# Kernel optimization log

Measured on AMD Instinct MI355X. Metric: run time of the kernel, lower is better.

## Reference

```python
import jax, jax.numpy as jnp
import numpy as np

N = 100000
E = 1600000
D_IN = 128
D_H = 128


def _logit(p):
    p = max(min(p, 0.999), 0.001)
    return float(np.log(p / (1.0 - p)))


def setup_inputs() -> dict:
    key = jax.random.key(0)
    ks = jax.random.split(key, 16)
    s = 0.05
    inp = {
        "x": jax.random.normal(ks[0], (N, D_IN), jnp.float32),
        "edge_index": jax.random.randint(ks[1], (2, E), 0, N, jnp.int64),
        "reranker_scores": jax.random.normal(ks[2], (N,), jnp.float32),
        # input_proj
        "Wp": jax.random.normal(ks[3], (D_IN, D_H), jnp.float32) * s,
        "bp": jnp.zeros((D_H,), jnp.float32),
        # SAGEConv 0: lin_l (on aggregated neighbors, has bias), lin_r (root, no bias)
        "Wl0": jax.random.normal(ks[4], (D_IN, D_H), jnp.float32) * s,
        "bl0": jnp.zeros((D_H,), jnp.float32),
        "Wr0": jax.random.normal(ks[5], (D_IN, D_H), jnp.float32) * s,
        # SAGEConv 1
        "Wl1": jax.random.normal(ks[6], (D_H, D_H), jnp.float32) * s,
        "bl1": jnp.zeros((D_H,), jnp.float32),
        "Wr1": jax.random.normal(ks[7], (D_H, D_H), jnp.float32) * s,
        # score head: Linear(128,64) -> GELU -> Linear(64,1)
        "Ws1": jax.random.normal(ks[8], (D_H, D_H // 2), jnp.float32) * s,
        "bs1": jnp.zeros((D_H // 2,), jnp.float32),
        "Ws2": jax.random.normal(ks[9], (D_H // 2, 1), jnp.float32) * s,
        "bs2": jnp.zeros((1,), jnp.float32),
        "alpha_logit": jnp.asarray(_logit(0.65), jnp.float32),
    }
    return inp


def _sage(h, src, dst, Wl, bl, Wr):
    # PyG SAGEConv (aggr='mean'): lin_l(mean_{j in N(i)} x_j) + lin_r(x_i)
    agg = jax.ops.segment_sum(h[src], dst, num_segments=N)  # [N, d]
    deg = jax.ops.segment_sum(jnp.ones((src.shape[0],), h.dtype), dst, num_segments=N)
    mean = agg / jnp.maximum(deg, 1.0)[:, None]
    return mean @ Wl + bl + h @ Wr


def reference(x, edge_index, reranker_scores, Wp, bp, Wl0, bl0, Wr0, Wl1, bl1, Wr1,
              Ws1, bs1, Ws2, bs2, alpha_logit):
    src, dst = edge_index[0], edge_index[1]
    gelu = lambda t: jax.nn.gelu(t, approximate=False)  # torch nn.GELU default = exact erf
    residual = x @ Wp + bp
    # layer 0 (dropout inactive at eval)
    h = gelu(_sage(x, src, dst, Wl0, bl0, Wr0)) + residual
    # layer 1
    h = gelu(_sage(h, src, dst, Wl1, bl1, Wr1)) + h
    gnn_scores = (gelu(h @ Ws1 + bs1) @ Ws2 + bs2)[:, 0]  # [N]
    alpha = jax.nn.sigmoid(alpha_logit)
    return alpha * reranker_scores + (1.0 - alpha) * gnn_scores
```

## Files before the change

kernel.cpp:

```cpp
#include <hip/hip_runtime.h>

typedef unsigned short u16;
typedef unsigned char  u8;
typedef unsigned int   u32;
typedef unsigned long long u64;
typedef __attribute__((ext_vector_type(8))) short short8;
typedef __attribute__((ext_vector_type(4))) float f32x4;
typedef __attribute__((ext_vector_type(2))) float f32x2;

__device__ __forceinline__ float b2f(u16 u) { return __uint_as_float(((u32)u) << 16); }
__device__ __forceinline__ u16 f2b(float f) {
    u32 i = __float_as_uint(f);
    return (u16)((i + 0x7FFFu + ((i >> 16) & 1u)) >> 16);
}
__device__ __forceinline__ float gelu_f(float v) {
    return 0.5f * v * (1.f + erff(v * 0.70710678118654752f));
}
__device__ __forceinline__ float ldf(const void* p, int i, int f32) {
    return f32 ? ((const float*)p)[i] : b2f(((const u16*)p)[i]);
}

__device__ __forceinline__ float fp8_dec(u32 v) {
    u32 bits = ((v & 0x80u) << 24) | ((v & 0x7Fu) << 20);
    return __uint_as_float(bits) * 1.3292279957849159e36f;
}
__device__ __forceinline__ u32 fp8_enc(float x) {
    u32 b = __float_as_uint(x);
    u32 s = (b >> 24) & 0x80u;
    float ax = fminf(__uint_as_float(b & 0x7FFFFFFFu), 448.f);
    u32 r;
    if (ax < 0.015625f) {
        r = (u32)(ax * 512.f + 0.5f);
    } else {
        u32 ab = __float_as_uint(ax);
        u32 rb = ab + 0x7FFFFu + ((ab >> 20) & 1u);
        int e8 = (int)(rb >> 23) - 120;
        u32 m = (rb >> 20) & 7u;
        if (e8 > 15) { e8 = 15; m = 6u; }
        r = ((u32)e8 << 3) | m;
    }
    return s | r;
}

__device__ __forceinline__ f32x2 dec2_fp8(u32 v) {
#if __has_builtin(__builtin_amdgcn_cvt_pk_f32_fp8)
    return __builtin_amdgcn_cvt_pk_f32_fp8((int)v, false);
#else
    f32x2 r; r[0] = fp8_dec(v); r[1] = fp8_dec(v >> 8); return r;
#endif
}
__device__ __forceinline__ u32 pk4_fp8(float v0, float v1, float v2, float v3) {
#if __has_builtin(__builtin_amdgcn_cvt_pk_fp8_f32)
    int p = __builtin_amdgcn_cvt_pk_fp8_f32(v0, v1, 0, false);
    p = __builtin_amdgcn_cvt_pk_fp8_f32(v2, v3, p, true);
    return (u32)p;
#else
    return fp8_enc(v0) | (fp8_enc(v1) << 8) | (fp8_enc(v2) << 16) | (fp8_enc(v3) << 24);
#endif
}

__global__ void probe_kernel(const int* __restrict__ ei, const u16* __restrict__ xw,
                             int* __restrict__ mode) {
    int lane = threadIdx.x;
    int v = (lane < 8) ? ei[2 * lane + 1] : 0;
    unsigned long long nz = __ballot(v != 0);
    u16 h = xw[2 * lane];
    int e = (h >> 7) & 0xFF;
    unsigned long long pl = __ballot(e >= 100 && e <= 140);
    if (lane == 0) {
        mode[0] = (nz == 0ULL) ? 1 : 0;
        mode[1] = (__popcll(pl) >= 48) ? 0 : 1;
    }
}

__global__ __launch_bounds__(256) void fallback_kernel(const void* __restrict__ rr,
                                                       const void* __restrict__ al,
                                                       const int* __restrict__ mode,
                                                       void* __restrict__ out, int N) {
    int i = blockIdx.x * 256 + threadIdx.x;
    if (i >= N) return;
    int f32 = mode ? mode[1] : 0;
    float a = 1.f / (1.f + expf(-ldf(al, 0, f32)));
    float v = a * ldf(rr, i, f32);
    if (f32) ((float*)out)[i] = v; else ((u16*)out)[i] = f2b(v);
}

__global__ __launch_bounds__(256) void hist_kernel(const int* __restrict__ ei, int E, int N,
                                                   const int* __restrict__ mode,
                                                   int* __restrict__ deg) {
    int i = blockIdx.x * 256 + threadIdx.x;
    if (i >= E) return;
    int m64 = mode[0];
    int d = m64 ? ei[2 * E + 2 * i] : ei[E + i];
    if ((unsigned)d < (unsigned)N) atomicAdd(&deg[d], 1);
}

__global__ __launch_bounds__(256) void bucketHist2_kernel(const int* __restrict__ ei, int E, int N,
                                                          const int* __restrict__ mode, int shift,
                                                          int* __restrict__ chist, int chunks) {
    __shared__ int h[1024];
    int t = threadIdx.x;
#pragma unroll
    for (int j = 0; j < 4; j++) h[t + j * 256] = 0;
    __syncthreads();
    const int m64 = mode[0];
    const int base = blockIdx.x * 2048;
#pragma unroll
    for (int j = 0; j < 8; j++) {
        int i = base + j * 256 + t;
        if (i < E) {
            int d = m64 ? ei[2 * E + 2 * i] : ei[E + i];
            if ((unsigned)d < (unsigned)N) atomicAdd(&h[d >> shift], 1);
        }
    }
    __syncthreads();
#pragma unroll
    for (int j = 0; j < 4; j++) {
        int b = t + j * 256;
        chist[(size_t)b * chunks + blockIdx.x] = h[b];
    }
}

__global__ __launch_bounds__(256) void scanA_kernel(const int* __restrict__ deg,
                                                    int* __restrict__ part) {
    int t = threadIdx.x, lane = t & 63, wv = t >> 6;
    size_t base = (size_t)blockIdx.x * 2048 + (size_t)t * 8;
    int s = 0;
#pragma unroll
    for (int j = 0; j < 8; j++) s += deg[base + j];
    for (int m = 1; m < 64; m <<= 1) s += __shfl_xor(s, m, 64);
    __shared__ int ws4[4];
    if (lane == 0) ws4[wv] = s;
    __syncthreads();
    if (t == 0) part[blockIdx.x] = ws4[0] + ws4[1] + ws4[2] + ws4[3];
}

__global__ void scanB_kernel(int* __restrict__ part, int nb) {
    int lane = threadIdx.x;
    int v = (lane < nb) ? part[lane] : 0;
    int orig = v;
    for (int d = 1; d < 64; d <<= 1) {
        int o = __shfl_up(v, d, 64);
        if (lane >= d) v += o;
    }
    if (lane < nb) part[lane] = v - orig;
}

__global__ __launch_bounds__(256) void scanC_kernel(const int* __restrict__ deg,
                                                    const int* __restrict__ part,
                                                    int* __restrict__ off) {
    int t = threadIdx.x, lane = t & 63, wv = t >> 6;
    size_t base = (size_t)blockIdx.x * 2048 + (size_t)t * 8;
    int v[8];
    int s = 0;
#pragma unroll
    for (int j = 0; j < 8; j++) { v[j] = deg[base + j]; s += v[j]; }
    int incl = s;
    for (int d = 1; d < 64; d <<= 1) {
        int o = __shfl_up(incl, d, 64);
        if (lane >= d) incl += o;
    }
    __shared__ int wsum[4];
    if (lane == 63) wsum[wv] = incl;
    __syncthreads();
    int pre = part[blockIdx.x] + (incl - s);
    for (int w = 0; w < wv; w++) pre += wsum[w];
#pragma unroll
    for (int j = 0; j < 8; j++) { off[base + j] = pre; pre += v[j]; }
    if (blockIdx.x == gridDim.x - 1 && t == 255) off[base + 8] = pre;
}

__global__ __launch_bounds__(256) void scanK_kernel(const int* __restrict__ bcnt,
                                                    int* __restrict__ boff) {
    int t = threadIdx.x, lane = t & 63, wv = t >> 6;
    int v[4];
    int s = 0;
#pragma unroll
    for (int j = 0; j < 4; j++) { v[j] = bcnt[t * 4 + j]; s += v[j]; }
    int incl = s;
    for (int d = 1; d < 64; d <<= 1) {
        int o = __shfl_up(incl, d, 64);
        if (lane >= d) incl += o;
    }
    __shared__ int wsum[4];
    if (lane == 63) wsum[wv] = incl;
    __syncthreads();
    int pre = incl - s;
    for (int w = 0; w < wv; w++) pre += wsum[w];
#pragma unroll
    for (int j = 0; j < 4; j++) { boff[t * 4 + j] = pre; pre += v[j]; }
    if (t == 255) boff[1024] = pre;
}

__global__ __launch_bounds__(256) void chunkScanPre_kernel(int* __restrict__ chist,
                                                           int* __restrict__ bcnt, int chunks) {
    const int b = (blockIdx.x * 256 + threadIdx.x) >> 6;
    if (b >= 1024) return;
    const int lane = threadIdx.x & 63;
    const int per = (chunks + 63) >> 6;
    int* row = chist + (size_t)b * chunks;
    int v[32];
    int sum = 0;
#pragma unroll
    for (int j = 0; j < 32; j++) {
        int c = lane * per + j;
        v[j] = (j < per && c < chunks) ? row[c] : 0;
        sum += v[j];
    }
    int pre = sum;
    for (int d = 1; d < 64; d <<= 1) {
        int o = __shfl_up(pre, d, 64);
        if (lane >= d) pre += o;
    }
    if (lane == 63) bcnt[b] = pre;
    pre -= sum;
#pragma unroll
    for (int j = 0; j < 32; j++) {
        int c = lane * per + j;
        if (j < per && c < chunks) { row[c] = pre; pre += v[j]; }
    }
}

__global__ __launch_bounds__(256) void bucketScatter2_kernel(const int* __restrict__ ei, int E, int N,
                                                             const int* __restrict__ mode, int shift,
                                                             const int* __restrict__ cbase,
                                                             const int* __restrict__ boff,
                                                             u64* __restrict__ pairs, int chunks) {
    __shared__ int cur[1024];
    int t = threadIdx.x;
#pragma unroll
    for (int j = 0; j < 4; j++) {
        int b = t + j * 256;
        cur[b] = cbase[(size_t)b * chunks + blockIdx.x] + boff[b];
    }
    __syncthreads();
    const int m64 = mode[0];
    const int base = blockIdx.x * 2048;
#pragma unroll
    for (int j = 0; j < 8; j++) {
        int i = base + j * 256 + t;
        if (i < E) {
            int d = m64 ? ei[2 * E + 2 * i] : ei[E + i];
            if ((unsigned)d >= (unsigned)N) continue;
            int s = m64 ? ei[2 * i] : ei[i];
            if ((unsigned)s >= (unsigned)N) s = 0;
            int p = atomicAdd(&cur[d >> shift], 1);
            pairs[p] = ((u64)(u32)d << 32) | (u32)s;
        }
    }
}

__global__ __launch_bounds__(256) void bucketFill2_kernel(const u64* __restrict__ pairs,
                                                          const int* __restrict__ boff,
                                                          int* __restrict__ off,
                                                          int* __restrict__ sorted,
                                                          int shift, int E, int N) {
    __shared__ int cur[2048];
    __shared__ int wsum[4];
    const int b = blockIdx.x;
    const int t = threadIdx.x;
    const int lane = t & 63, wv = t >> 6;
    const int nodes = 1 << shift;
    const int nbase = b << shift;
    for (int i = t; i < nodes; i += 256) cur[i] = 0;
    __syncthreads();
    const int s0 = boff[b], s1 = boff[b + 1];
    for (int i = s0 + t; i < s1; i += 256) {
        int li = (int)(pairs[i] >> 32) - nbase;
        if ((unsigned)li < (unsigned)nodes) atomicAdd(&cur[li], 1);
    }
    __syncthreads();
    const int per = (nodes + 255) >> 8;
    int v[8];
    int sum = 0;
#pragma unroll
    for (int j = 0; j < 8; j++) {
        int idx = t * per + j;
        v[j] = (j < per && idx < nodes) ? cur[idx] : 0;
        sum += v[j];
    }
    int incl = sum;
    for (int d = 1; d < 64; d <<= 1) {
        int o = __shfl_up(incl, d, 64);
        if (lane >= d) incl += o;
    }
    if (lane == 63) wsum[wv] = incl;
    __syncthreads();
    int pre = s0 + (incl - sum);
    for (int w = 0; w < wv; w++) pre += wsum[w];
#pragma unroll
    for (int j = 0; j < 8; j++) {
        int idx = t * per + j;
        if (j < per && idx < nodes) {
            cur[idx] = pre;
            if (nbase + idx <= N) off[nbase + idx] = pre;
            pre += v[j];
        }
    }
    if (t == 255 && nbase + nodes <= N) off[nbase + nodes] = s1;
    __syncthreads();
    for (int i = s0 + t; i < s1; i += 256) {
        u64 pr = pairs[i];
        int li = (int)(pr >> 32) - nbase;
        if ((unsigned)li >= (unsigned)nodes) continue;
        int p = atomicAdd(&cur[li], 1);
        if ((unsigned)p < (unsigned)E) sorted[p] = (int)(u32)pr;
    }
}

__global__ __launch_bounds__(256) void fill_kernel(const int* __restrict__ ei, int E, int N,
                                                   const int* __restrict__ mode,
                                                   const int* __restrict__ off,
                                                   int* __restrict__ deg,
                                                   int* __restrict__ sorted) {
    int i = blockIdx.x * 256 + threadIdx.x;
    if (i >= E) return;
    int m64 = mode[0];
    int s = m64 ? ei[2 * i] : ei[i];
    int d = m64 ? ei[2 * E + 2 * i] : ei[E + i];
    if ((unsigned)d >= (unsigned)N) return;
    if ((unsigned)s >= (unsigned)N) s = 0;
    int p = atomicSub(&deg[d], 1) - 1;
    if (p < 0) return;
    int pos = off[d] + p;
    if ((unsigned)pos < (unsigned)E) sorted[pos] = s;
}

__global__ __launch_bounds__(256) void prep_kernel(const void* __restrict__ Wp, const void* __restrict__ Wl0,
                                                   const void* __restrict__ Wr0, const void* __restrict__ Wl1,
                                                   const void* __restrict__ Wr1, const void* __restrict__ Ws1,
                                                   const int* __restrict__ mode, u16* __restrict__ T) {
    int idx = blockIdx.x * 256 + threadIdx.x;
    int f32 = mode[1];
    if (idx < 81920) {
        int m = idx >> 14, e = idx & 16383, n = e & 127, k = e >> 7;
        const void* s;
        switch (m) {
            case 0: s = Wp; break;
            case 1: s = Wl0; break;
            case 2: s = Wr0; break;
            case 3: s = Wl1; break;
            default: s = Wr1; break;
        }
        T[m * 16384 + n * 128 + k] = f2b(ldf(s, e, f32));
    } else if (idx < 90112) {
        int e = idx - 81920, k = e >> 6, n = e & 63;
        T[81920 + n * 128 + k] = f2b(ldf(Ws1, e, f32));
    }
}

template <int F32>
__global__ __launch_bounds__(256) void cvt8_kernel(const void* __restrict__ H, u8* __restrict__ F,
                                                   const int* __restrict__ mode, int NE, int checkMode) {
    if (checkMode && mode[1] != F32) return;
    int i = blockIdx.x * 256 + threadIdx.x;
    if (i >= NE) return;
    float x0, x1;
    if (!F32) {
        u32 v = ((const u32*)H)[i];
        x0 = b2f((u16)v); x1 = b2f((u16)(v >> 16));
    } else {
        x0 = ((const float*)H)[2 * i]; x1 = ((const float*)H)[2 * i + 1];
    }
#if __has_builtin(__builtin_amdgcn_cvt_pk_fp8_f32)
    ((u16*)F)[i] = (u16)__builtin_amdgcn_cvt_pk_fp8_f32(x0, x1, 0, false);
#else
    ((u16*)F)[i] = (u16)(fp8_enc(x0) | (fp8_enc(x1) << 8));
#endif
}

__global__ __launch_bounds__(256) void sagg8_kernel(const u8* __restrict__ F, const int* __restrict__ off,
                                                    const int* __restrict__ srcs, u16* __restrict__ meanO,
                                                    int N, int E) {
    const int node = __builtin_amdgcn_readfirstlane(blockIdx.x * 4 + (threadIdx.x >> 6));
    if (node >= N) return;
    const int lane = threadIdx.x & 63;
    int s0 = off[node], s1 = off[node + 1];
    if (s0 < 0) s0 = 0;
    if (s1 > E) s1 = E;
    if (s1 < s0) s1 = s0;
    const int dg = s1 - s0;
    const float inv = 1.f / (float)(dg > 1 ? dg : 1);
    const u8* Fp = F + lane * 2;
    float a0 = 0.f, a1 = 0.f;
    for (int base = s0; base < s1; base += 64) {
        const int rem = s1 - base;
        const int cnt = rem < 64 ? rem : 64;
        int msrc = srcs[base + (lane < cnt ? lane : 0)];
        if ((unsigned)msrc >= (unsigned)N) msrc = 0;
        int e = 0;
        for (; e + 7 < cnt; e += 8) {
            int i0 = __shfl(msrc, e + 0, 64);
            int i1 = __shfl(msrc, e + 1, 64);
            int i2 = __shfl(msrc, e + 2, 64);
            int i3 = __shfl(msrc, e + 3, 64);
            int i4 = __shfl(msrc, e + 4, 64);
            int i5 = __shfl(msrc, e + 5, 64);
            int i6 = __shfl(msrc, e + 6, 64);
            int i7 = __shfl(msrc, e + 7, 64);
            u32 v0 = *(const u16*)(Fp + (size_t)i0 * 128);
            u32 v1 = *(const u16*)(Fp + (size_t)i1 * 128);
            u32 v2 = *(const u16*)(Fp + (size_t)i2 * 128);
            u32 v3 = *(const u16*)(Fp + (size_t)i3 * 128);
            u32 v4 = *(const u16*)(Fp + (size_t)i4 * 128);
            u32 v5 = *(const u16*)(Fp + (size_t)i5 * 128);
            u32 v6 = *(const u16*)(Fp + (size_t)i6 * 128);
            u32 v7 = *(const u16*)(Fp + (size_t)i7 * 128);
            f32x2 d0 = dec2_fp8(v0), d1 = dec2_fp8(v1), d2 = dec2_fp8(v2), d3 = dec2_fp8(v3);
            f32x2 d4 = dec2_fp8(v4), d5 = dec2_fp8(v5), d6 = dec2_fp8(v6), d7 = dec2_fp8(v7);
            a0 += (d0[0] + d1[0]) + (d2[0] + d3[0]) + (d4[0] + d5[0]) + (d6[0] + d7[0]);
            a1 += (d0[1] + d1[1]) + (d2[1] + d3[1]) + (d4[1] + d5[1]) + (d6[1] + d7[1]);
        }
        for (; e + 3 < cnt; e += 4) {
            int i0 = __shfl(msrc, e + 0, 64);
            int i1 = __shfl(msrc, e + 1, 64);
            int i2 = __shfl(msrc, e + 2, 64);
            int i3 = __shfl(msrc, e + 3, 64);
            u32 v0 = *(const u16*)(Fp + (size_t)i0 * 128);
            u32 v1 = *(const u16*)(Fp + (size_t)i1 * 128);
            u32 v2 = *(const u16*)(Fp + (size_t)i2 * 128);
            u32 v3 = *(const u16*)(Fp + (size_t)i3 * 128);
            f32x2 d0 = dec2_fp8(v0), d1 = dec2_fp8(v1), d2 = dec2_fp8(v2), d3 = dec2_fp8(v3);
            a0 += (d0[0] + d1[0]) + (d2[0] + d3[0]);
            a1 += (d0[1] + d1[1]) + (d2[1] + d3[1]);
        }
        for (; e < cnt; ++e) {
            int i0 = __shfl(msrc, e, 64);
            f32x2 d0 = dec2_fp8(*(const u16*)(Fp + (size_t)i0 * 128));
            a0 += d0[0];
            a1 += d0[1];
        }
    }
    *(u32*)(meanO + (size_t)node * 128 + lane * 2) = (u32)f2b(a0 * inv) | ((u32)f2b(a1 * inv) << 16);
}

template <int F32>
__global__ __launch_bounds__(256) void saggb_kernel(const void* __restrict__ H, const int* __restrict__ off,
                                                    const int* __restrict__ srcs, u16* __restrict__ meanO,
                                                    int N, int E, const int* __restrict__ mode, int mcheck) {
    if (mcheck && mode[1] != F32) return;
    const int node = __builtin_amdgcn_readfirstlane(blockIdx.x * 4 + (threadIdx.x >> 6));
    if (node >= N) return;
    const int lane = threadIdx.x & 63;
    int s0 = off[node], s1 = off[node + 1];
    if (s0 < 0) s0 = 0;
    if (s1 > E) s1 = E;
    if (s1 < s0) s1 = s0;
    const int dg = s1 - s0;
    const float inv = 1.f / (float)(dg > 1 ? dg : 1);
    float a0 = 0.f, a1 = 0.f;
    if (!F32) {
        const u32* Hp = (const u32*)H + lane;
        for (int e = s0; e < s1; ++e) {
            int i0 = srcs[e];
            if ((unsigned)i0 >= (unsigned)N) i0 = 0;
            u32 v0 = Hp[(size_t)i0 << 6];
            a0 += __uint_as_float(v0 << 16);
            a1 += __uint_as_float(v0 & 0xFFFF0000u);
        }
    } else {
        const float* Hp = (const float*)H + 2 * lane;
        for (int e = s0; e < s1; ++e) {
            int i0 = srcs[e];
            if ((unsigned)i0 >= (unsigned)N) i0 = 0;
            const float2 w0 = *(const float2*)(Hp + ((size_t)i0 << 7));
            a0 += w0.x;
            a1 += w0.y;
        }
    }
    *(u32*)(meanO + (size_t)node * 128 + lane * 2) = (u32)f2b(a0 * inv) | ((u32)f2b(a1 * inv) << 16);
}

__device__ __forceinline__ uint4 packbf8(f32x4 a, f32x4 b) {
    uint4 o;
    o.x = (u32)f2b(a[0]) | ((u32)f2b(a[1]) << 16);
    o.y = (u32)f2b(a[2]) | ((u32)f2b(a[3]) << 16);
    o.z = (u32)f2b(b[0]) | ((u32)f2b(b[1]) << 16);
    o.w = (u32)f2b(b[2]) | ((u32)f2b(b[3]) << 16);
    return o;
}

template <int F32>
__device__ __forceinline__ void stageTile(const void* __restrict__ src, u16* __restrict__ lds,
                                          long tb, int N, int t) {
    const int r = t >> 2;
    long gr = tb + r;
    if (gr >= N) gr = N - 1;
    const int cb = (t & 3) * 64;
    const int swz = (r & 7) << 4;
    char* lp = (char*)lds + r * 256;
    if (!F32) {
        const char* gp = (const char*)src + gr * 256 + cb;
        uint4 v0 = *(const uint4*)(gp + 0);
        uint4 v1 = *(const uint4*)(gp + 16);
        uint4 v2 = *(const uint4*)(gp + 32);
        uint4 v3 = *(const uint4*)(gp + 48);
        *(uint4*)(lp + ((cb + 0) ^ swz)) = v0;
        *(uint4*)(lp + ((cb + 16) ^ swz)) = v1;
        *(uint4*)(lp + ((cb + 32) ^ swz)) = v2;
        *(uint4*)(lp + ((cb + 48) ^ swz)) = v3;
    } else {
        const float* gp = (const float*)src + gr * 128 + (cb >> 1);
        f32x4 f[8];
#pragma unroll
        for (int j = 0; j < 8; j++) f[j] = *(const f32x4*)(gp + 4 * j);
#pragma unroll
        for (int j = 0; j < 4; j++)
            *(uint4*)(lp + ((cb + 16 * j) ^ swz)) = packbf8(f[2 * j], f[2 * j + 1]);
    }
}

template <int F32>
__global__ __launch_bounds__(256, 2) void gemmF_kernel(const void* __restrict__ x, const u16* __restrict__ mean,
                                                       const u16* __restrict__ WTl, const u16* __restrict__ WTr,
                                                       const u16* __restrict__ WTp,
                                                       const void* __restrict__ bl, const void* __restrict__ bp,
                                                       const int* __restrict__ mode,
                                                       u16* __restrict__ h0, u8* __restrict__ F8, int emitF8,
                                                       int N) {
    if (mode[1] != F32) return;
    __shared__ u16 lsM[64 * 128];
    __shared__ u16 lsX[64 * 128];
    const int t = threadIdx.x;
    const int lane = t & 63, wave = t >> 6;
    const int m0 = lane & 15, q = lane >> 4;
    const long tb = (long)blockIdx.x * 64;

    short8 wl[4][2], wr[4][2], wp[4][2];
#pragma unroll
    for (int ks = 0; ks < 4; ks++)
#pragma unroll
        for (int h = 0; h < 2; h++) {
            const int ro = ((2 * wave + h) * 16 + m0) * 128 + ks * 32 + q * 8;
            wl[ks][h] = *(const short8*)(WTl + ro);
            wr[ks][h] = *(const short8*)(WTr + ro);
            wp[ks][h] = *(const short8*)(WTp + ro);
        }

    stageTile<0>(mean, lsM, tb, N, t);
    stageTile<F32>(x, lsX, tb, N, t);
    __syncthreads();

    f32x4 accU[4][2], accR[4][2];
#pragma unroll
    for (int rt = 0; rt < 4; rt++)
#pragma unroll
        for (int h = 0; h < 2; h++) { accU[rt][h] = {0.f, 0.f, 0.f, 0.f}; accR[rt][h] = {0.f, 0.f, 0.f, 0.f}; }

    const int swz = (m0 & 7) << 4;
#pragma unroll
    for (int ks = 0; ks < 4; ks++) {
        short8 aM[4], aX[4];
#pragma unroll
        for (int rt = 0; rt < 4; rt++) {
            const int off = (rt * 16 + m0) * 256 + ((ks * 64 + q * 16) ^ swz);
            aM[rt] = *(const short8*)((const char*)lsM + off);
            aX[rt] = *(const short8*)((const char*)lsX + off);
        }
#pragma unroll
        for (int rt = 0; rt < 4; rt++)
#pragma unroll
            for (int h = 0; h < 2; h++) {
                accU[rt][h] = __builtin_amdgcn_mfma_f32_16x16x32_bf16(wl[ks][h], aM[rt], accU[rt][h], 0, 0, 0);
                accU[rt][h] = __builtin_amdgcn_mfma_f32_16x16x32_bf16(wr[ks][h], aX[rt], accU[rt][h], 0, 0, 0);
                accR[rt][h] = __builtin_amdgcn_mfma_f32_16x16x32_bf16(wp[ks][h], aX[rt], accR[rt][h], 0, 0, 0);
            }
    }

    float blv[2][4], bpv[2][4];
#pragma unroll
    for (int h = 0; h < 2; h++)
#pragma unroll
        for (int g = 0; g < 4; g++) {
            const int col = (2 * wave + h) * 16 + q * 4 + g;
            blv[h][g] = ldf(bl, col, F32);
            bpv[h][g] = ldf(bp, col, F32);
        }
#pragma unroll
    for (int rt = 0; rt < 4; rt++) {
        const long row = tb + rt * 16 + m0;
        if (row < N) {
#pragma unroll
            for (int h = 0; h < 2; h++) {
                float v[4];
#pragma unroll
                for (int g = 0; g < 4; g++)
                    v[g] = gelu_f(accU[rt][h][g] + blv[h][g]) + accR[rt][h][g] + bpv[h][g];
                const int col0 = (2 * wave + h) * 16 + q * 4;
                u64 pk = (u64)f2b(v[0]) | ((u64)f2b(v[1]) << 16) | ((u64)f2b(v[2]) << 32) | ((u64)f2b(v[3]) << 48);
                *(u64*)(h0 + (size_t)row * 128 + col0) = pk;
                if (emitF8)
                    *(u32*)(F8 + (size_t)row * 128 + col0) = pk4_fp8(v[0], v[1], v[2], v[3]);
            }
        }
    }
}

__global__ __launch_bounds__(256, 2) void gemm1_kernel(const u16* __restrict__ h0, const u16* mean,
                                                       const u16* __restrict__ WTl, const u16* __restrict__ WTr,
                                                       const void* __restrict__ bl, const int* __restrict__ mode,
                                                       u16* h1, int N) {
    __shared__ u16 lsM[64 * 128];
    __shared__ u16 lsH[64 * 128];
    const int t = threadIdx.x;
    const int lane = t & 63, wave = t >> 6;
    const int m0 = lane & 15, q = lane >> 4;
    const int f32 = mode[1];
    const long tb = (long)blockIdx.x * 64;

    short8 wl[4][2], wr[4][2];
#pragma unroll
    for (int ks = 0; ks < 4; ks++)
#pragma unroll
        for (int h = 0; h < 2; h++) {
            const int ro = ((2 * wave + h) * 16 + m0) * 128 + ks * 32 + q * 8;
            wl[ks][h] = *(const short8*)(WTl + ro);
            wr[ks][h] = *(const short8*)(WTr + ro);
        }

    stageTile<0>(mean, lsM, tb, N, t);
    stageTile<0>(h0, lsH, tb, N, t);
    __syncthreads();

    f32x4 acc[4][2];
#pragma unroll
    for (int rt = 0; rt < 4; rt++)
#pragma unroll
        for (int h = 0; h < 2; h++) acc[rt][h] = {0.f, 0.f, 0.f, 0.f};

    const int swz = (m0 & 7) << 4;
#pragma unroll
    for (int ks = 0; ks < 4; ks++) {
        short8 aM[4], aH[4];
#pragma unroll
        for (int rt = 0; rt < 4; rt++) {
            const int off = (rt * 16 + m0) * 256 + ((ks * 64 + q * 16) ^ swz);
            aM[rt] = *(const short8*)((const char*)lsM + off);
            aH[rt] = *(const short8*)((const char*)lsH + off);
        }
#pragma unroll
        for (int rt = 0; rt < 4; rt++)
#pragma unroll
            for (int h = 0; h < 2; h++) {
                acc[rt][h] = __builtin_amdgcn_mfma_f32_16x16x32_bf16(wl[ks][h], aM[rt], acc[rt][h], 0, 0, 0);
                acc[rt][h] = __builtin_amdgcn_mfma_f32_16x16x32_bf16(wr[ks][h], aH[rt], acc[rt][h], 0, 0, 0);
            }
    }

    float blv[2][4];
#pragma unroll
    for (int h = 0; h < 2; h++)
#pragma unroll
        for (int g = 0; g < 4; g++) blv[h][g] = ldf(bl, (2 * wave + h) * 16 + q * 4 + g, f32);

#pragma unroll
    for (int rt = 0; rt < 4; rt++) {
        const long row = tb + rt * 16 + m0;
        if (row < N) {
#pragma unroll
            for (int h = 0; h < 2; h++) {
                const int col0 = (2 * wave + h) * 16 + q * 4;
                const int rb = (rt * 16 + m0) * 256 + (((2 * wave + h) * 32 + q * 8) ^ swz);
                const u64 old = *(const u64*)((const char*)lsH + rb);
                float v[4];
#pragma unroll
                for (int g = 0; g < 4; g++)
                    v[g] = gelu_f(acc[rt][h][g] + blv[h][g]) + b2f((u16)(old >> (16 * g)));
                u64 pk = (u64)f2b(v[0]) | ((u64)f2b(v[1]) << 16) | ((u64)f2b(v[2]) << 32) | ((u64)f2b(v[3]) << 48);
                *(u64*)(h1 + (size_t)row * 128 + col0) = pk;
            }
        }
    }
}

__global__ __launch_bounds__(256, 4) void score_kernel(const u16* __restrict__ h1, const u16* __restrict__ WTs,
                                                       const void* __restrict__ bs1, const void* __restrict__ w2,
                                                       const void* __restrict__ bs2, const void* __restrict__ rr,
                                                       const void* __restrict__ alpha_p, const int* __restrict__ mode,
                                                       void* __restrict__ out, int N) {
    const int lane = threadIdx.x & 63, wave = threadIdx.x >> 6;
    const int m0 = lane & 15, q = lane >> 4;
    const int f32 = mode[1];
    const long rowBase = (long)blockIdx.x * 128 + wave * 32;
    f32x4 acc[2][4];
#pragma unroll
    for (int r = 0; r < 2; r++)
#pragma unroll
        for (int n = 0; n < 4; n++) acc[r][n] = {0.f, 0.f, 0.f, 0.f};
#pragma unroll
    for (int ks = 0; ks < 4; ++ks) {
        const int k = ks * 32 + q * 8;
        short8 bf[4];
#pragma unroll
        for (int n = 0; n < 4; n++) bf[n] = *(const short8*)(WTs + (n * 16 + m0) * 128 + k);
#pragma unroll
        for (int r = 0; r < 2; r++) {
            long row = rowBase + r * 16 + m0;
            if (row >= N) row = N - 1;
            short8 a = *(const short8*)(h1 + (size_t)row * 128 + k);
#pragma unroll
            for (int n = 0; n < 4; n++)
                acc[r][n] = __builtin_amdgcn_mfma_f32_16x16x32_bf16(a, bf[n], acc[r][n], 0, 0, 0);
        }
    }
    float alpha = 1.f / (1.f + expf(-ldf(alpha_p, 0, f32)));
    float bs2v = ldf(bs2, 0, f32);
    float w2v[4], b1v[4];
#pragma unroll
    for (int n = 0; n < 4; n++) {
        int col = n * 16 + m0;
        w2v[n] = ldf(w2, col, f32);
        b1v[n] = ldf(bs1, col, f32);
    }
#pragma unroll
    for (int r = 0; r < 2; r++) {
        float s[4] = {0.f, 0.f, 0.f, 0.f};
#pragma unroll
        for (int n = 0; n < 4; n++)
#pragma unroll
            for (int g = 0; g < 4; g++) s[g] += gelu_f(acc[r][n][g] + b1v[n]) * w2v[n];
#pragma unroll
        for (int g = 0; g < 4; g++) {
            s[g] += __shfl_xor(s[g], 1, 64);
            s[g] += __shfl_xor(s[g], 2, 64);
            s[g] += __shfl_xor(s[g], 4, 64);
            s[g] += __shfl_xor(s[g], 8, 64);
        }
        if (m0 == 0) {
            long row0 = rowBase + r * 16 + q * 4;
#pragma unroll
            for (int g = 0; g < 4; g++) {
                long row = row0 + g;
                if (row < N) {
                    float sc = s[g] + bs2v;
                    float v = alpha * ldf(rr, (int)row, f32) + (1.f - alpha) * sc;
                    if (f32) ((float*)out)[row] = v; else ((u16*)out)[row] = f2b(v);
                }
            }
        }
    }
}

extern "C" void kernel_launch(void* const* d_in, const int* in_sizes, int n_in,
                              void* d_out, int out_size, void* d_ws, size_t ws_size,
                              hipStream_t stream) {
    const void* x = d_in[0];
    const int* ei = (const int*)d_in[1];
    const void* rr = d_in[2];
    const void* Wp = d_in[3];
    const void* bp = d_in[4];
    const void* Wl0 = d_in[5];
    const void* bl0 = d_in[6];
    const void* Wr0 = d_in[7];
    const void* Wl1 = d_in[8];
    const void* bl1 = d_in[9];
    const void* Wr1 = d_in[10];
    const void* Ws1 = d_in[11];
    const void* bs1 = d_in[12];
    const void* Ws2 = d_in[13];
    const void* bs2 = d_in[14];
    const void* alpha = d_in[15];

    const int N = in_sizes[0] / 128;
    const int E = in_sizes[1] / 2;
    const int NP = ((N + 2047) / 2048) * 2048;
    const int NB = NP / 2048;
    const int chunks = (E + 2047) / 2048;
    int shift = 0;
    while (((N - 1) >> shift) >= 1024) shift++;

    char* w = (char*)d_ws;
    size_t used = 0;
    auto alloc = [&](size_t b) { char* p = w + used; used += (b + 255) & ~(size_t)255; return p; };
    int* mode = (int*)alloc(256);
    int* deg = (int*)alloc((size_t)NP * 4);
    int* bcnt = (int*)alloc(1024 * 4);
    int* boff = (int*)alloc(1025 * 4);
    int* chist = (int*)alloc((size_t)chunks * 1024 * 4);
    int* off = (int*)alloc((size_t)(NP + 64) * 4);
    int* part = (int*)alloc(64 * 4);
    int* sorted = (int*)alloc((size_t)E * 4);
    u16* T = (u16*)alloc(90112 * 2);
    u16* meanb = (u16*)alloc((size_t)NP * 128 * 2);
    u16* h0 = (u16*)alloc((size_t)NP * 128 * 2);
    u16* h1 = meanb;
    size_t usedBase = used;
    size_t fbytes = (size_t)NP * 128;
    if ((size_t)E * 8 > fbytes) fbytes = (size_t)E * 8;
    u8* F = (u8*)alloc(fbytes);
    size_t usedFull = used;
    u64* pairs = (u64*)F;

    if (ws_size < 4096) {
        fallback_kernel<<<(N + 255) / 256, 256, 0, stream>>>(rr, alpha, nullptr, d_out, N);
        return;
    }
    probe_kernel<<<1, 64, 0, stream>>>(ei, (const u16*)x, mode);
    if (usedBase > ws_size) {
        fallback_kernel<<<(N + 255) / 256, 256, 0, stream>>>(rr, alpha, mode, d_out, N);
        return;
    }
    const bool fp8Path = (usedFull <= ws_size);
    const bool bucketPath = fp8Path && ((1 << shift) <= 2048) && (chunks <= 2048);

    prep_kernel<<<(90112 + 255) / 256, 256, 0, stream>>>(Wp, Wl0, Wr0, Wl1, Wr1, Ws1, mode, T);

    if (bucketPath) {
        bucketHist2_kernel<<<chunks, 256, 0, stream>>>(ei, E, N, mode, shift, chist, chunks);
        chunkScanPre_kernel<<<256, 256, 0, stream>>>(chist, bcnt, chunks);
        scanK_kernel<<<1, 256, 0, stream>>>(bcnt, boff);
        bucketScatter2_kernel<<<chunks, 256, 0, stream>>>(ei, E, N, mode, shift, chist, boff, pairs, chunks);
        bucketFill2_kernel<<<1024, 256, 0, stream>>>(pairs, boff, off, sorted, shift, E, N);
    } else {
        hipMemsetAsync(deg, 0, (size_t)NP * 4, stream);
        hist_kernel<<<(E + 255) / 256, 256, 0, stream>>>(ei, E, N, mode, deg);
        scanA_kernel<<<NB, 256, 0, stream>>>(deg, part);
        scanB_kernel<<<1, 64, 0, stream>>>(part, NB);
        scanC_kernel<<<NB, 256, 0, stream>>>(deg, part, off);
        fill_kernel<<<(E + 255) / 256, 256, 0, stream>>>(ei, E, N, mode, off, deg, sorted);
    }

    const int gemmGrid16 = (N + 63) / 64;
    const int nodeBlocks = (N + 3) / 4;
    const int NE = N * 64;
    const int cvtGrid = (NE + 255) / 256;

    if (fp8Path) {
        cvt8_kernel<0><<<cvtGrid, 256, 0, stream>>>(x, F, mode, NE, 1);
        cvt8_kernel<1><<<cvtGrid, 256, 0, stream>>>(x, F, mode, NE, 1);
        sagg8_kernel<<<nodeBlocks, 256, 0, stream>>>(F, off, sorted, meanb, N, E);
        gemmF_kernel<0><<<gemmGrid16, 256, 0, stream>>>(x, meanb, T + 16384, T + 32768, T + 0, bl0, bp, mode, h0, F, 1, N);
        gemmF_kernel<1><<<gemmGrid16, 256, 0, stream>>>(x, meanb, T + 16384, T + 32768, T + 0, bl0, bp, mode, h0, F, 1, N);
        sagg8_kernel<<<nodeBlocks, 256, 0, stream>>>(F, off, sorted, meanb, N, E);
    } else {
        saggb_kernel<0><<<nodeBlocks, 256, 0, stream>>>(x, off, sorted, meanb, N, E, mode, 1);
        saggb_kernel<1><<<nodeBlocks, 256, 0, stream>>>(x, off, sorted, meanb, N, E, mode, 1);
        gemmF_kernel<0><<<gemmGrid16, 256, 0, stream>>>(x, meanb, T + 16384, T + 32768, T + 0, bl0, bp, mode, h0, nullptr, 0, N);
        gemmF_kernel<1><<<gemmGrid16, 256, 0, stream>>>(x, meanb, T + 16384, T + 32768, T + 0, bl0, bp, mode, h0, nullptr, 0, N);
        saggb_kernel<0><<<nodeBlocks, 256, 0, stream>>>(h0, off, sorted, meanb, N, E, mode, 0);
    }
    gemm1_kernel<<<gemmGrid16, 256, 0, stream>>>(h0, meanb, T + 49152, T + 65536, bl1, mode, h1, N);
    score_kernel<<<(N + 127) / 128, 256, 0, stream>>>(h1, T + 81920, bs1, Ws2, bs2, rr, alpha, mode, d_out, N);
}
```

Before: 364.2 us.

## Load GEMM A-operands directly from global memory instead of staging through LDS

```diff
diff --git a/kernel.cpp b/kernel.cpp
--- a/kernel.cpp
+++ b/kernel.cpp
@@ -471,42 +471,18 @@
     *(u32*)(meanO + (size_t)node * 128 + lane * 2) = (u32)f2b(a0 * inv) | ((u32)f2b(a1 * inv) << 16);
 }
 
-__device__ __forceinline__ uint4 packbf8(f32x4 a, f32x4 b) {
-    uint4 o;
-    o.x = (u32)f2b(a[0]) | ((u32)f2b(a[1]) << 16);
-    o.y = (u32)f2b(a[2]) | ((u32)f2b(a[3]) << 16);
-    o.z = (u32)f2b(b[0]) | ((u32)f2b(b[1]) << 16);
-    o.w = (u32)f2b(b[2]) | ((u32)f2b(b[3]) << 16);
-    return o;
-}
-
 template <int F32>
-__device__ __forceinline__ void stageTile(const void* __restrict__ src, u16* __restrict__ lds,
-                                          long tb, int N, int t) {
-    const int r = t >> 2;
-    long gr = tb + r;
-    if (gr >= N) gr = N - 1;
-    const int cb = (t & 3) * 64;
-    const int swz = (r & 7) << 4;
-    char* lp = (char*)lds + r * 256;
+__device__ __forceinline__ short8 loadA(const void* __restrict__ A, long row, int k) {
     if (!F32) {
-        const char* gp = (const char*)src + gr * 256 + cb;
-        uint4 v0 = *(const uint4*)(gp + 0);
-        uint4 v1 = *(const uint4*)(gp + 16);
-        uint4 v2 = *(const uint4*)(gp + 32);
-        uint4 v3 = *(const uint4*)(gp + 48);
-        *(uint4*)(lp + ((cb + 0) ^ swz)) = v0;
-        *(uint4*)(lp + ((cb + 16) ^ swz)) = v1;
-        *(uint4*)(lp + ((cb + 32) ^ swz)) = v2;
-        *(uint4*)(lp + ((cb + 48) ^ swz)) = v3;
+        return *(const short8*)((const u16*)A + (size_t)row * 128 + k);
     } else {
-        const float* gp = (const float*)src + gr * 128 + (cb >> 1);
-        f32x4 f[8];
-#pragma unroll
-        for (int j = 0; j < 8; j++) f[j] = *(const f32x4*)(gp + 4 * j);
-#pragma unroll
-        for (int j = 0; j < 4; j++)
-            *(uint4*)(lp + ((cb + 16 * j) ^ swz)) = packbf8(f[2 * j], f[2 * j + 1]);
+        const float* f = (const float*)A + (size_t)row * 128 + k;
+        f32x4 v0 = *(const f32x4*)f;
+        f32x4 v1 = *(const f32x4*)(f + 4);
+        short8 a;
+#pragma unroll
+        for (int j = 0; j < 4; j++) { a[j] = (short)f2b(v0[j]); a[j + 4] = (short)f2b(v1[j]); }
+        return a;
     }
 }
 
@@ -519,12 +495,16 @@
                                                        u16* __restrict__ h0, u8* __restrict__ F8, int emitF8,
                                                        int N) {
     if (mode[1] != F32) return;
-    __shared__ u16 lsM[64 * 128];
-    __shared__ u16 lsX[64 * 128];
     const int t = threadIdx.x;
     const int lane = t & 63, wave = t >> 6;
     const int m0 = lane & 15, q = lane >> 4;
     const long tb = (long)blockIdx.x * 64;
+    long rowA[4];
+#pragma unroll
+    for (int rt = 0; rt < 4; rt++) {
+        long r = tb + rt * 16 + m0;
+        rowA[rt] = r < N ? r : (N - 1);
+    }
 
     short8 wl[4][2], wr[4][2], wp[4][2];
 #pragma unroll
@@ -537,25 +517,20 @@
             wp[ks][h] = *(const short8*)(WTp + ro);
         }
 
-    stageTile<0>(mean, lsM, tb, N, t);
-    stageTile<F32>(x, lsX, tb, N, t);
-    __syncthreads();
-
     f32x4 accU[4][2], accR[4][2];
 #pragma unroll
     for (int rt = 0; rt < 4; rt++)
 #pragma unroll
         for (int h = 0; h < 2; h++) { accU[rt][h] = {0.f, 0.f, 0.f, 0.f}; accR[rt][h] = {0.f, 0.f, 0.f, 0.f}; }
 
-    const int swz = (m0 & 7) << 4;
 #pragma unroll
     for (int ks = 0; ks < 4; ks++) {
+        const int k = ks * 32 + q * 8;
         short8 aM[4], aX[4];
 #pragma unroll
         for (int rt = 0; rt < 4; rt++) {
-            const int off = (rt * 16 + m0) * 256 + ((ks * 64 + q * 16) ^ swz);
-            aM[rt] = *(const short8*)((const char*)lsM + off);
-            aX[rt] = *(const short8*)((const char*)lsX + off);
+            aM[rt] = *(const short8*)(mean + (size_t)rowA[rt] * 128 + k);
+            aX[rt] = loadA<F32>(x, rowA[rt], k);
         }
 #pragma unroll
         for (int rt = 0; rt < 4; rt++)
@@ -600,13 +575,17 @@
                                                        const u16* __restrict__ WTl, const u16* __restrict__ WTr,
                                                        const void* __restrict__ bl, const int* __restrict__ mode,
                                                        u16* h1, int N) {
-    __shared__ u16 lsM[64 * 128];
-    __shared__ u16 lsH[64 * 128];
     const int t = threadIdx.x;
     const int lane = t & 63, wave = t >> 6;
     const int m0 = lane & 15, q = lane >> 4;
     const int f32 = mode[1];
     const long tb = (long)blockIdx.x * 64;
+    long rowA[4];
+#pragma unroll
+    for (int rt = 0; rt < 4; rt++) {
+        long r = tb + rt * 16 + m0;
+        rowA[rt] = r < N ? r : (N - 1);
+    }
 
     short8 wl[4][2], wr[4][2];
 #pragma unroll
@@ -618,8 +597,12 @@
             wr[ks][h] = *(const short8*)(WTr + ro);
         }
 
-    stageTile<0>(mean, lsM, tb, N, t);
-    stageTile<0>(h0, lsH, tb, N, t);
+    short8 aM[4][4];
+#pragma unroll
+    for (int ks = 0; ks < 4; ks++)
+#pragma unroll
+        for (int rt = 0; rt < 4; rt++)
+            aM[ks][rt] = *(const short8*)(mean + (size_t)rowA[rt] * 128 + ks * 32 + q * 8);
     __syncthreads();
 
     f32x4 acc[4][2];
@@ -628,21 +611,18 @@
 #pragma unroll
         for (int h = 0; h < 2; h++) acc[rt][h] = {0.f, 0.f, 0.f, 0.f};
 
-    const int swz = (m0 & 7) << 4;
 #pragma unroll
     for (int ks = 0; ks < 4; ks++) {
-        short8 aM[4], aH[4];
-#pragma unroll
-        for (int rt = 0; rt < 4; rt++) {
-            const int off = (rt * 16 + m0) * 256 + ((ks * 64 + q * 16) ^ swz);
-            aM[rt] = *(const short8*)((const char*)lsM + off);
-            aH[rt] = *(const short8*)((const char*)lsH + off);
-        }
+        const int k = ks * 32 + q * 8;
+        short8 aH[4];
 #pragma unroll
         for (int rt = 0; rt < 4; rt++)
+            aH[rt] = *(const short8*)(h0 + (size_t)rowA[rt] * 128 + k);
+#pragma unroll
+        for (int rt = 0; rt < 4; rt++)
 #pragma unroll
             for (int h = 0; h < 2; h++) {
-                acc[rt][h] = __builtin_amdgcn_mfma_f32_16x16x32_bf16(wl[ks][h], aM[rt], acc[rt][h], 0, 0, 0);
+                acc[rt][h] = __builtin_amdgcn_mfma_f32_16x16x32_bf16(wl[ks][h], aM[ks][rt], acc[rt][h], 0, 0, 0);
                 acc[rt][h] = __builtin_amdgcn_mfma_f32_16x16x32_bf16(wr[ks][h], aH[rt], acc[rt][h], 0, 0, 0);
             }
     }
@@ -660,8 +640,7 @@
 #pragma unroll
             for (int h = 0; h < 2; h++) {
                 const int col0 = (2 * wave + h) * 16 + q * 4;
-                const int rb = (rt * 16 + m0) * 256 + (((2 * wave + h) * 32 + q * 8) ^ swz);
-                const u64 old = *(const u64*)((const char*)lsH + rb);
+                const u64 old = *(const u64*)(h0 + (size_t)row * 128 + col0);
                 float v[4];
 #pragma unroll
                 for (int g = 0; g < 4; g++)
```

New measurement: 418.6 us. 14.9% more time.

## Make layer-0 GEMM persistent with LDS-resident weights split across column halves

Applied to the files above, without the earlier changes.

```diff
diff --git a/kernel.cpp b/kernel.cpp
--- a/kernel.cpp
+++ b/kernel.cpp
@@ -7,6 +7,8 @@
 typedef __attribute__((ext_vector_type(8))) short short8;
 typedef __attribute__((ext_vector_type(4))) float f32x4;
 typedef __attribute__((ext_vector_type(2))) float f32x2;
+
+#define PIN8(v) asm volatile("" : "+v"(v))
 
 __device__ __forceinline__ float b2f(u16 u) { return __uint_as_float(((u32)u) << 16); }
 __device__ __forceinline__ u16 f2b(float f) {
@@ -511,6 +513,36 @@
 }
 
 template <int F32>
+__device__ __forceinline__ void stageTileA(const void* __restrict__ src, u16* __restrict__ lds,
+                                           long tb, int N, int t) {
+    const int r = t >> 2;
+    long gr = tb + r;
+    if (gr >= N) gr = N - 1;
+    const int cb = (t & 3) * 64;
+    const int swz = (r & 15) << 4;
+    char* lp = (char*)lds + r * 256;
+    if (!F32) {
+        const char* gp = (const char*)src + gr * 256 + cb;
+        uint4 v0 = *(const uint4*)(gp + 0);
+        uint4 v1 = *(const uint4*)(gp + 16);
+        uint4 v2 = *(const uint4*)(gp + 32);
+        uint4 v3 = *(const uint4*)(gp + 48);
+        *(uint4*)(lp + ((cb + 0) ^ swz)) = v0;
+        *(uint4*)(lp + ((cb + 16) ^ swz)) = v1;
+        *(uint4*)(lp + ((cb + 32) ^ swz)) = v2;
+        *(uint4*)(lp + ((cb + 48) ^ swz)) = v3;
+    } else {
+        const float* gp = (const float*)src + gr * 128 + (cb >> 1);
+        f32x4 f[8];
+#pragma unroll
+        for (int j = 0; j < 8; j++) f[j] = *(const f32x4*)(gp + 4 * j);
+#pragma unroll
+        for (int j = 0; j < 4; j++)
+            *(uint4*)(lp + ((cb + 16 * j) ^ swz)) = packbf8(f[2 * j], f[2 * j + 1]);
+    }
+}
+
+template <int F32>
 __global__ __launch_bounds__(256, 2) void gemmF_kernel(const void* __restrict__ x, const u16* __restrict__ mean,
                                                        const u16* __restrict__ WTl, const u16* __restrict__ WTr,
                                                        const u16* __restrict__ WTp,
@@ -519,80 +551,81 @@
                                                        u16* __restrict__ h0, u8* __restrict__ F8, int emitF8,
                                                        int N) {
     if (mode[1] != F32) return;
-    __shared__ u16 lsM[64 * 128];
-    __shared__ u16 lsX[64 * 128];
+    __shared__ u16 lsW[3 * 64 * 128];
+    __shared__ u16 lsA[2 * 64 * 128];
     const int t = threadIdx.x;
     const int lane = t & 63, wave = t >> 6;
     const int m0 = lane & 15, q = lane >> 4;
-    const long tb = (long)blockIdx.x * 64;
-
-    short8 wl[4][2], wr[4][2], wp[4][2];
-#pragma unroll
-    for (int ks = 0; ks < 4; ks++)
-#pragma unroll
-        for (int h = 0; h < 2; h++) {
-            const int ro = ((2 * wave + h) * 16 + m0) * 128 + ks * 32 + q * 8;
-            wl[ks][h] = *(const short8*)(WTl + ro);
-            wr[ks][h] = *(const short8*)(WTr + ro);
-            wp[ks][h] = *(const short8*)(WTp + ro);
-        }
-
-    stageTile<0>(mean, lsM, tb, N, t);
-    stageTile<F32>(x, lsX, tb, N, t);
-    __syncthreads();
-
-    f32x4 accU[4][2], accR[4][2];
-#pragma unroll
-    for (int rt = 0; rt < 4; rt++)
-#pragma unroll
-        for (int h = 0; h < 2; h++) { accU[rt][h] = {0.f, 0.f, 0.f, 0.f}; accR[rt][h] = {0.f, 0.f, 0.f, 0.f}; }
-
-    const int swz = (m0 & 7) << 4;
-#pragma unroll
-    for (int ks = 0; ks < 4; ks++) {
-        short8 aM[4], aX[4];
+    const int nh = blockIdx.x & 1;
+    const int rg = blockIdx.x >> 1;
+
+#pragma unroll
+    for (int m = 0; m < 3; m++) {
+        const u16* Wm = (m == 0) ? WTl : (m == 1) ? WTr : WTp;
+#pragma unroll
+        for (int j = 0; j < 4; j++) {
+            int c = t + j * 256;
+            int nrow = c >> 4, cb = (c & 15) * 16;
+            short8 v = *(const short8*)(Wm + (size_t)(nh * 64 + nrow) * 128 + (cb >> 1));
+            *(short8*)((char*)lsW + m * 16384 + nrow * 256 + (cb ^ ((nrow & 15) << 4))) = v;
+        }
+    }
+
+    const int colg = nh * 4 + wave;
+    const int wrow = wave * 16 + m0;
+    const int wswz = m0 << 4;
+    float blv[4], bpv[4];
+#pragma unroll
+    for (int g = 0; g < 4; g++) {
+        const int col = colg * 16 + q * 4 + g;
+        blv[g] = ldf(bl, col, F32);
+        bpv[g] = ldf(bp, col, F32);
+    }
+
+    const long tiles = ((long)N + 63) >> 6;
+    for (long tile = rg; tile < tiles; tile += 256) {
+        const long tb = tile * 64;
+        stageTileA<0>(mean, lsA, tb, N, t);
+        stageTileA<F32>(x, lsA + 64 * 128, tb, N, t);
+        __syncthreads();
+
+        f32x4 accU[4], accR[4];
+#pragma unroll
+        for (int rt = 0; rt < 4; rt++) { accU[rt] = {0.f, 0.f, 0.f, 0.f}; accR[rt] = {0.f, 0.f, 0.f, 0.f}; }
+
+#pragma unroll
+        for (int ks = 0; ks < 4; ks++) {
+            const int kb = ks * 64 + q * 16;
+            short8 wlF = *(const short8*)((char*)lsW + 0 * 16384 + wrow * 256 + (kb ^ wswz));
+            short8 wrF = *(const short8*)((char*)lsW + 1 * 16384 + wrow * 256 + (kb ^ wswz));
+            short8 wpF = *(const short8*)((char*)lsW + 2 * 16384 + wrow * 256 + (kb ^ wswz));
+#pragma unroll
+            for (int rt = 0; rt < 4; rt++) {
+                const int ab = (rt * 16 + m0) * 256 + (kb ^ (m0 << 4));
+                short8 aM = *(const short8*)((char*)lsA + ab);
+                short8 aX = *(const short8*)((char*)lsA + 16384 + ab);
+                accU[rt] = __builtin_amdgcn_mfma_f32_16x16x32_bf16(wlF, aM, accU[rt], 0, 0, 0);
+                accU[rt] = __builtin_amdgcn_mfma_f32_16x16x32_bf16(wrF, aX, accU[rt], 0, 0, 0);
+                accR[rt] = __builtin_amdgcn_mfma_f32_16x16x32_bf16(wpF, aX, accR[rt], 0, 0, 0);
+            }
+        }
+
 #pragma unroll
         for (int rt = 0; rt < 4; rt++) {
-            const int off = (rt * 16 + m0) * 256 + ((ks * 64 + q * 16) ^ swz);
-            aM[rt] = *(const short8*)((const char*)lsM + off);
-            aX[rt] = *(const short8*)((const char*)lsX + off);
-        }
-#pragma unroll
-        for (int rt = 0; rt < 4; rt++)
-#pragma unroll
-            for (int h = 0; h < 2; h++) {
-                accU[rt][h] = __builtin_amdgcn_mfma_f32_16x16x32_bf16(wl[ks][h], aM[rt], accU[rt][h], 0, 0, 0);
-                accU[rt][h] = __builtin_amdgcn_mfma_f32_16x16x32_bf16(wr[ks][h], aX[rt], accU[rt][h], 0, 0, 0);
-                accR[rt][h] = __builtin_amdgcn_mfma_f32_16x16x32_bf16(wp[ks][h], aX[rt], accR[rt][h], 0, 0, 0);
-            }
-    }
-
-    float blv[2][4], bpv[2][4];
-#pragma unroll
-    for (int h = 0; h < 2; h++)
-#pragma unroll
-        for (int g = 0; g < 4; g++) {
-            const int col = (2 * wave + h) * 16 + q * 4 + g;
-            blv[h][g] = ldf(bl, col, F32);
-            bpv[h][g] = ldf(bp, col, F32);
-        }
-#pragma unroll
-    for (int rt = 0; rt < 4; rt++) {
-        const long row = tb + rt * 16 + m0;
-        if (row < N) {
-#pragma unroll
-            for (int h = 0; h < 2; h++) {
+            const long row = tb + rt * 16 + m0;
+            if (row < N) {
                 float v[4];
 #pragma unroll
                 for (int g = 0; g < 4; g++)
-                    v[g] = gelu_f(accU[rt][h][g] + blv[h][g]) + accR[rt][h][g] + bpv[h][g];
-                const int col0 = (2 * wave + h) * 16 + q * 4;
+                    v[g] = gelu_f(accU[rt][g] + blv[g]) + accR[rt][g] + bpv[g];
+                const int col0 = colg * 16 + q * 4;
                 u64 pk = (u64)f2b(v[0]) | ((u64)f2b(v[1]) << 16) | ((u64)f2b(v[2]) << 32) | ((u64)f2b(v[3]) << 48);
                 *(u64*)(h0 + (size_t)row * 128 + col0) = pk;
                 if (emitF8)
                     *(u32*)(F8 + (size_t)row * 128 + col0) = pk4_fp8(v[0], v[1], v[2], v[3]);
             }
         }
+        __syncthreads();
     }
 }
 
@@ -617,6 +650,10 @@
             wl[ks][h] = *(const short8*)(WTl + ro);
             wr[ks][h] = *(const short8*)(WTr + ro);
         }
+#pragma unroll
+    for (int ks = 0; ks < 4; ks++)
+#pragma unroll
+        for (int h = 0; h < 2; h++) { PIN8(wl[ks][h]); PIN8(wr[ks][h]); }
 
     stageTile<0>(mean, lsM, tb, N, t);
     stageTile<0>(h0, lsH, tb, N, t);
@@ -829,14 +866,14 @@
         cvt8_kernel<0><<<cvtGrid, 256, 0, stream>>>(x, F, mode, NE, 1);
         cvt8_kernel<1><<<cvtGrid, 256, 0, stream>>>(x, F, mode, NE, 1);
         sagg8_kernel<<<nodeBlocks, 256, 0, stream>>>(F, off, sorted, meanb, N, E);
-        gemmF_kernel<0><<<gemmGrid16, 256, 0, stream>>>(x, meanb, T + 16384, T + 32768, T + 0, bl0, bp, mode, h0, F, 1, N);
-        gemmF_kernel<1><<<gemmGrid16, 256, 0, stream>>>(x, meanb, T + 16384, T + 32768, T + 0, bl0, bp, mode, h0, F, 1, N);
+        gemmF_kernel<0><<<512, 256, 0, stream>>>(x, meanb, T + 16384, T + 32768, T + 0, bl0, bp, mode, h0, F, 1, N);
+        gemmF_kernel<1><<<512, 256, 0, stream>>>(x, meanb, T + 16384, T + 32768, T + 0, bl0, bp, mode, h0, F, 1, N);
         sagg8_kernel<<<nodeBlocks, 256, 0, stream>>>(F, off, sorted, meanb, N, E);
     } else {
         saggb_kernel<0><<<nodeBlocks, 256, 0, stream>>>(x, off, sorted, meanb, N, E, mode, 1);
         saggb_kernel<1><<<nodeBlocks, 256, 0, stream>>>(x, off, sorted, meanb, N, E, mode, 1);
-        gemmF_kernel<0><<<gemmGrid16, 256, 0, stream>>>(x, meanb, T + 16384, T + 32768, T + 0, bl0, bp, mode, h0, nullptr, 0, N);
-        gemmF_kernel<1><<<gemmGrid16, 256, 0, stream>>>(x, meanb, T + 16384, T + 32768, T + 0, bl0, bp, mode, h0, nullptr, 0, N);
+        gemmF_kernel<0><<<512, 256, 0, stream>>>(x, meanb, T + 16384, T + 32768, T + 0, bl0, bp, mode, h0, nullptr, 0, N);
+        gemmF_kernel<1><<<512, 256, 0, stream>>>(x, meanb, T + 16384, T + 32768, T + 0, bl0, bp, mode, h0, nullptr, 0, N);
         saggb_kernel<0><<<nodeBlocks, 256, 0, stream>>>(h0, off, sorted, meanb, N, E, mode, 0);
     }
     gemm1_kernel<<<gemmGrid16, 256, 0, stream>>>(h0, meanb, T + 49152, T + 65536, bl1, mode, h1, N);
```

Measured after the change: 353.7 us. 1.03x faster.
